# Kernel tuning notes

Measured on AMD Instinct MI355X. Metric: run time of the kernel, lower is better.

Reference implementation:

```python
import jax, jax.numpy as jnp
import numpy as np

K = 1.0      # spring constant
R0 = 1.0     # equilibrium bond length
EPS = 1e-20  # division guard
NUM_GRAPHS = 64


def setup_inputs() -> dict:
    key = jax.random.key(0)
    k1, k2, k3 = jax.random.split(key, 3)
    N, E = 100000, 3200000
    pos = jax.random.normal(k1, (N, 3), dtype=jnp.float32)
    edge_index = jax.random.randint(k2, (2, E), 0, N, dtype=jnp.int64)
    batch = jnp.sort(jax.random.randint(k3, (N,), 0, NUM_GRAPHS, dtype=jnp.int64))
    return {"pos": pos, "edge_index": edge_index, "batch": batch}


def reference(pos, edge_index, batch):
    i, j = edge_index[0], edge_index[1]
    dr = pos[i] - pos[j]                       # (E, 3)
    d = jnp.linalg.norm(dr, axis=1)            # (E,)
    delta = d - R0
    edge_energy = 0.5 * K * delta ** 2         # (E,)
    energy = jax.ops.segment_sum(edge_energy, batch[i], num_segments=NUM_GRAPHS)
    direction = dr / (d + EPS)[:, None]        # (E, 3)
    force_contrib = (K * delta)[:, None] * direction
    forces = jnp.zeros_like(pos).at[i].add(-force_contrib).at[j].add(force_contrib)
    return energy, forces
```

## Files before the change

### kernel.cpp

```cpp
#include <hip/hip_runtime.h>

#define NUM_GRAPHS 64
#define NSC 160
#define SCN 625
#define XPAD 628
#define SB 512
#define CAP 128
#define SEGSTRIDE (NSC * CAP)
#define PBREC 12800
#define BITER 8
#define FSCALE 32768.0f
#define FINV   (1.0f / 32768.0f)

__global__ __launch_bounds__(1024, 8) void bin_kernel(
    const float* __restrict__ pos, const int* __restrict__ batch,
    float4* __restrict__ pos4, float* __restrict__ energy,
    const int* __restrict__ ei,
    unsigned int* __restrict__ recs,
    int* __restrict__ counts,
    int N, int E, int per_block)
{
    __shared__ unsigned int buf[PBREC];
    __shared__ int hist[NSC];
    __shared__ int csr[NSC];
    __shared__ int cursor[NSC];
    __shared__ int scan_s[NSC];

    const int t = threadIdx.x, b = blockIdx.x;
    const int lane = t & 63, w = t >> 6;
    const int e0 = b * per_block, e1 = min(E, e0 + per_block);

    {
        const int gt = b * 1024 + t;
        if (gt < N) {
            float4 v;
            v.x = pos[3 * gt + 0];
            v.y = pos[3 * gt + 1];
            v.z = pos[3 * gt + 2];
            v.w = __int_as_float(batch[gt]);
            pos4[gt] = v;
        }
        if (b == 0 && t < NUM_GRAPHS) energy[t] = 0.f;
    }

    int civ[BITER], cjv[BITER];

    for (int i = t; i < NSC; i += 1024) hist[i] = 0;
    __syncthreads();

    #pragma unroll
    for (int it = 0; it < BITER; ++it) {
        const int e = e0 + t + it * 1024;
        if (e < e1) {
            const int iv = ei[e], jv = ei[E + e];
            civ[it] = iv; cjv[it] = jv;
            atomicAdd(&hist[iv / SCN], 1);
            atomicAdd(&hist[jv / SCN], 1);
        }
    }
    __syncthreads();

    if (t < NSC) scan_s[t] = hist[t];
    __syncthreads();
    for (int d = 1; d < NSC; d <<= 1) {
        int v = 0;
        if (t < NSC && t >= d) v = scan_s[t - d];
        __syncthreads();
        if (t < NSC) scan_s[t] += v;
        __syncthreads();
    }
    if (t < NSC) {
        const int excl = scan_s[t] - hist[t];
        csr[t] = excl;
        cursor[t] = excl;
    }
    __syncthreads();

    #pragma unroll
    for (int it = 0; it < BITER; ++it) {
        const int e = e0 + t + it * 1024;
        if (e < e1) {
            const int iv = civ[it], jv = cjv[it];
            const int si = iv / SCN, sj = jv / SCN;
            const int s1 = atomicAdd(&cursor[si], 1);
            buf[s1] = (unsigned int)(iv - si * SCN) | ((unsigned int)jv << 10) | (1u << 27);
            const int s2 = atomicAdd(&cursor[sj], 1);
            buf[s2] = (unsigned int)(jv - sj * SCN) | ((unsigned int)iv << 10);
        }
    }
    __syncthreads();

    unsigned int* dst0 = recs + (size_t)b * NSC * CAP;
    for (int s = w; s < NSC; s += 16) {
        const int base = csr[s];
        const int cnt  = min(hist[s], CAP);
        for (int k = lane; k < cnt; k += 64)
            dst0[s * CAP + k] = buf[base + k];
        if (lane == 0) counts[b * NSC + s] = cnt;
    }
}

template<int G>
__global__ __launch_bounds__(256, 8) void accumulate_kernel(
    const float4* __restrict__ pos4,
    const unsigned int* __restrict__ recs,
    const int* __restrict__ counts,
    float* __restrict__ energy,
    int* __restrict__ xpart,
    unsigned long long* __restrict__ yzpart)
{
    __shared__ float4 slab[SCN];
    __shared__ __align__(16) int facc_x[XPAD];
    __shared__ __align__(16) unsigned long long facc_yz[XPAD];
    __shared__ float ered[8];

    const int t    = threadIdx.x;
    const int lane = t & 63;
    const int w    = t >> 6;
    const int s    = blockIdx.x % NSC;
    const int g    = blockIdx.x / NSC;

    constexpr int SPB   = SB / G;
    constexpr int SPW   = SPB / 4;
    constexpr int NPASS = (SPW + 7) / 8;

    for (int i = t; i < SCN; i += 256) slab[i] = pos4[s * SCN + i];
    for (int i = 4 * t; i < XPAD; i += 1024) {
        int4 z = {0, 0, 0, 0};
        *(int4*)&facc_x[i] = z;
    }
    for (int i = 4 * t; i < 2 * XPAD; i += 1024) {
        int4 z = {0, 0, 0, 0};
        *(int4*)&((int*)facc_yz)[i] = z;
    }
    __syncthreads();

    const int gmin_i = __float_as_int(slab[0].w);
    float e_lo = 0.f, e_hi = 0.f;

    for (int pass = 0; pass < NPASS; ++pass) {
        const int seg0 = g * SPB + w * SPW + pass * 8;
        int v = (lane < 8) ? counts[(seg0 + lane) * NSC + s] : 0;
        #pragma unroll
        for (int d = 1; d < 8; d <<= 1) {
            const int u = __shfl_up(v, d);
            if (lane >= d) v += u;
        }
        const int b0 = __shfl(v, 0), b1 = __shfl(v, 1), b2 = __shfl(v, 2),
                  b3 = __shfl(v, 3), b4 = __shfl(v, 4), b5 = __shfl(v, 5),
                  b6 = __shfl(v, 6);
        const int tot = __shfl(v, 7);
        const unsigned int* bp = recs + ((size_t)seg0 * NSC + s) * CAP;

        for (int base = 0; base < tot; base += 256) {
            unsigned int rec[4];
            bool  val[4];
            int   a[4];
            float4 pb[4];
            #pragma unroll
            for (int u = 0; u < 4; ++u) {
                const int r = base + lane + (u << 6);
                val[u] = r < tot;
                if (val[u]) {
                    const int k = (r >= b0) + (r >= b1) + (r >= b2) + (r >= b3)
                                + (r >= b4) + (r >= b5) + (r >= b6);
                    int prev = 0;
                    prev = (k > 0) ? b0 : prev; prev = (k > 1) ? b1 : prev;
                    prev = (k > 2) ? b2 : prev; prev = (k > 3) ? b3 : prev;
                    prev = (k > 4) ? b4 : prev; prev = (k > 5) ? b5 : prev;
                    prev = (k > 6) ? b6 : prev;
                    rec[u] = bp[(size_t)k * SEGSTRIDE + (r - prev)];
                }
            }
            #pragma unroll
            for (int u = 0; u < 4; ++u) {
                if (val[u]) {
                    a[u]  = (int)(rec[u] & 1023);
                    pb[u] = pos4[(rec[u] >> 10) & 0x1FFFF];
                }
            }
            #pragma unroll
            for (int u = 0; u < 4; ++u) {
                if (val[u]) {
                    const float4 pa = slab[a[u]];
                    const float dx = pa.x - pb[u].x;
                    const float dy = pa.y - pb[u].y;
                    const float dz = pa.z - pb[u].z;
                    const float r2  = fmaxf(dx*dx + dy*dy + dz*dz, 1e-24f);
                    const float inv = __builtin_amdgcn_rsqf(r2);
                    const float sc  = 1.0f - inv;
                    const int xq = __float2int_rn(-sc * dx * FSCALE);
                    const int yq = __float2int_rn(-sc * dy * FSCALE);
                    const int zq = __float2int_rn(-sc * dz * FSCALE);
                    atomicAdd(&facc_x[a[u]], xq);
                    const unsigned long long pk =
                        ((unsigned long long)(unsigned int)zq << 32)
                        + (unsigned long long)(unsigned int)yq;
                    atomicAdd(&facc_yz[a[u]], pk);
                    if (rec[u] >> 27) {
                        const float delta = r2 * inv - 1.0f;
                        const float e = 0.5f * delta * delta;
                        if (__float_as_int(pa.w) == gmin_i) e_lo += e;
                        else                                e_hi += e;
                    }
                }
            }
        }
    }

    #pragma unroll
    for (int d = 32; d > 0; d >>= 1) {
        e_lo += __shfl_down(e_lo, d);
        e_hi += __shfl_down(e_hi, d);
    }
    if (lane == 0) { ered[2 * w] = e_lo; ered[2 * w + 1] = e_hi; }

    __syncthreads();
    int* xdst = xpart + (size_t)(s * G + g) * XPAD;
    unsigned long long* zdst = yzpart + (size_t)(s * G + g) * XPAD;
    for (int i = t; i < SCN; i += 256) xdst[i] = facc_x[i];
    for (int i = t; i < SCN; i += 256) zdst[i] = facc_yz[i];
    if (t == 0)
        atomicAdd(&energy[__float_as_int(slab[0].w)],
                  ered[0] + ered[2] + ered[4] + ered[6]);
    if (t == 1)
        atomicAdd(&energy[__float_as_int(slab[SCN - 1].w)],
                  ered[1] + ered[3] + ered[5] + ered[7]);
}

template<int G>
__global__ __launch_bounds__(256) void reduce_kernel(
    const int* __restrict__ xpart,
    const unsigned long long* __restrict__ yzpart,
    float* __restrict__ forces, int N)
{
    const int n = blockIdx.x * 256 + threadIdx.x;
    if (n >= N) return;
    const int s = n / SCN, a = n - s * SCN;
    int sx = 0, sy = 0, sz = 0;
    #pragma unroll
    for (int g = 0; g < G; ++g) {
        const size_t p = (size_t)(s * G + g) * XPAD + a;
        sx += xpart[p];
        const unsigned long long v = yzpart[p];
        sy += (int)(unsigned int)(v & 0xffffffffull);
        sz += (int)(unsigned int)(v >> 32);
    }
    forces[3 * n + 0] = (float)sx * FINV;
    forces[3 * n + 1] = (float)sy * FINV;
    forces[3 * n + 2] = (float)sz * FINV;
}

extern "C" void kernel_launch(void* const* d_in, const int* in_sizes, int n_in,
                              void* d_out, int out_size, void* d_ws, size_t ws_size,
                              hipStream_t stream) {
    const float* pos   = (const float*)d_in[0];
    const int*   ei    = (const int*)d_in[1];
    const int*   batch = (const int*)d_in[2];

    const int E = in_sizes[1] / 2;
    const int N = in_sizes[0] / 3;

    float* energy = (float*)d_out;
    float* forces = (float*)d_out + NUM_GRAPHS;

    const int per_block = (E + SB - 1) / SB;

    char* w = (char*)d_ws;
    float4* pos4 = (float4*)w;
    size_t off = (size_t)N * 16;
    unsigned int* recs = (unsigned int*)(w + off);
    off += (size_t)SB * NSC * CAP * 4;
    int* counts = (int*)(w + off);
    off += (size_t)SB * NSC * 4;
    int* xpart = (int*)(w + off);
    const size_t xbytes16 = (size_t)NSC * 16 * XPAD * 4;
    const size_t xbytes8  = (size_t)NSC * 8  * XPAD * 4;

    bin_kernel<<<SB, 1024, 0, stream>>>(pos, batch, pos4, energy,
                                        ei, recs, counts, N, E, per_block);

    const size_t need16 = off + xbytes16 + (size_t)NSC * 16 * XPAD * 8;
    if (ws_size >= need16) {
        unsigned long long* yzpart = (unsigned long long*)((char*)xpart + xbytes16);
        accumulate_kernel<16><<<NSC * 16, 256, 0, stream>>>(
            pos4, recs, counts, energy, xpart, yzpart);
        reduce_kernel<16><<<(N + 255) / 256, 256, 0, stream>>>(
            xpart, yzpart, forces, N);
    } else {
        unsigned long long* yzpart = (unsigned long long*)((char*)xpart + xbytes8);
        accumulate_kernel<8><<<NSC * 8, 256, 0, stream>>>(
            pos4, recs, counts, energy, xpart, yzpart);
        reduce_kernel<8><<<(N + 255) / 256, 256, 0, stream>>>(
            xpart, yzpart, forces, N);
    }
}
```

Baseline: 142.7 us.

## Replace per-group force partials with global atomic accumulation

Each accumulate block now atomically adds its fixed-point force tile into a single global per-node buffer, which the bin kernel zeroes. This replaces writing G partial slabs and summing them in a separate reduce kernel. The final pass becomes a simple coalesced convert over 3N outputs. In exchange it adds global atomic contention (16 groups per node) and always uses G=16 without the workspace-size fallback.

```diff
diff --git a/kernel.cpp b/kernel.cpp
--- a/kernel.cpp
+++ b/kernel.cpp
@@ -15,6 +15,8 @@
 __global__ __launch_bounds__(1024, 8) void bin_kernel(
     const float* __restrict__ pos, const int* __restrict__ batch,
     float4* __restrict__ pos4, float* __restrict__ energy,
+    int* __restrict__ gx,
+    unsigned long long* __restrict__ gyz,
     const int* __restrict__ ei,
     unsigned int* __restrict__ recs,
     int* __restrict__ counts,
@@ -39,6 +41,8 @@
             v.z = pos[3 * gt + 2];
             v.w = __int_as_float(batch[gt]);
             pos4[gt] = v;
+            gx[gt] = 0;
+            gyz[gt] = 0ull;
         }
         if (b == 0 && t < NUM_GRAPHS) energy[t] = 0.f;
     }
@@ -106,8 +110,8 @@
     const unsigned int* __restrict__ recs,
     const int* __restrict__ counts,
     float* __restrict__ energy,
-    int* __restrict__ xpart,
-    unsigned long long* __restrict__ yzpart)
+    int* __restrict__ gx,
+    unsigned long long* __restrict__ gyz)
 {
     __shared__ float4 slab[SCN];
     __shared__ __align__(16) int facc_x[XPAD];
@@ -216,10 +220,8 @@
     if (lane == 0) { ered[2 * w] = e_lo; ered[2 * w + 1] = e_hi; }
 
     __syncthreads();
-    int* xdst = xpart + (size_t)(s * G + g) * XPAD;
-    unsigned long long* zdst = yzpart + (size_t)(s * G + g) * XPAD;
-    for (int i = t; i < SCN; i += 256) xdst[i] = facc_x[i];
-    for (int i = t; i < SCN; i += 256) zdst[i] = facc_yz[i];
+    for (int i = t; i < SCN; i += 256) atomicAdd(&gx[s * SCN + i], facc_x[i]);
+    for (int i = t; i < SCN; i += 256) atomicAdd(&gyz[s * SCN + i], facc_yz[i]);
     if (t == 0)
         atomicAdd(&energy[__float_as_int(slab[0].w)],
                   ered[0] + ered[2] + ered[4] + ered[6]);
@@ -228,27 +230,19 @@
                   ered[1] + ered[3] + ered[5] + ered[7]);
 }
 
-template<int G>
-__global__ __launch_bounds__(256) void reduce_kernel(
-    const int* __restrict__ xpart,
-    const unsigned long long* __restrict__ yzpart,
+__global__ __launch_bounds__(256) void convert_kernel(
+    const int* __restrict__ gx,
+    const unsigned long long* __restrict__ gyz,
     float* __restrict__ forces, int N)
 {
-    const int n = blockIdx.x * 256 + threadIdx.x;
-    if (n >= N) return;
-    const int s = n / SCN, a = n - s * SCN;
-    int sx = 0, sy = 0, sz = 0;
-    #pragma unroll
-    for (int g = 0; g < G; ++g) {
-        const size_t p = (size_t)(s * G + g) * XPAD + a;
-        sx += xpart[p];
-        const unsigned long long v = yzpart[p];
-        sy += (int)(unsigned int)(v & 0xffffffffull);
-        sz += (int)(unsigned int)(v >> 32);
-    }
-    forces[3 * n + 0] = (float)sx * FINV;
-    forces[3 * n + 1] = (float)sy * FINV;
-    forces[3 * n + 2] = (float)sz * FINV;
+    const int idx = blockIdx.x * 256 + threadIdx.x;
+    if (idx >= 3 * N) return;
+    const int n = idx / 3, c = idx - 3 * n;
+    int v;
+    if (c == 0)      v = gx[n];
+    else if (c == 1) v = (int)(unsigned int)(gyz[n] & 0xffffffffull);
+    else             v = (int)(unsigned int)(gyz[n] >> 32);
+    forces[idx] = (float)v * FINV;
 }
 
 extern "C" void kernel_launch(void* const* d_in, const int* in_sizes, int n_in,
@@ -273,25 +267,16 @@
     off += (size_t)SB * NSC * CAP * 4;
     int* counts = (int*)(w + off);
     off += (size_t)SB * NSC * 4;
-    int* xpart = (int*)(w + off);
-    const size_t xbytes16 = (size_t)NSC * 16 * XPAD * 4;
-    const size_t xbytes8  = (size_t)NSC * 8  * XPAD * 4;
-
-    bin_kernel<<<SB, 1024, 0, stream>>>(pos, batch, pos4, energy,
+    int* gx = (int*)(w + off);
+    off += (size_t)N * 4;
+    unsigned long long* gyz = (unsigned long long*)(w + off);
+
+    bin_kernel<<<SB, 1024, 0, stream>>>(pos, batch, pos4, energy, gx, gyz,
                                         ei, recs, counts, N, E, per_block);
 
-    const size_t need16 = off + xbytes16 + (size_t)NSC * 16 * XPAD * 8;
-    if (ws_size >= need16) {
-        unsigned long long* yzpart = (unsigned long long*)((char*)xpart + xbytes16);
-        accumulate_kernel<16><<<NSC * 16, 256, 0, stream>>>(
-            pos4, recs, counts, energy, xpart, yzpart);
-        reduce_kernel<16><<<(N + 255) / 256, 256, 0, stream>>>(
-            xpart, yzpart, forces, N);
-    } else {
-        unsigned long long* yzpart = (unsigned long long*)((char*)xpart + xbytes8);
-        accumulate_kernel<8><<<NSC * 8, 256, 0, stream>>>(
-            pos4, recs, counts, energy, xpart, yzpart);
-        reduce_kernel<8><<<(N + 255) / 256, 256, 0, stream>>>(
-            xpart, yzpart, forces, N);
-    }
-}
+    accumulate_kernel<16><<<NSC * 16, 256, 0, stream>>>(
+        pos4, recs, counts, energy, gx, gyz);
+
+    convert_kernel<<<(3 * N + 255) / 256, 256, 0, stream>>>(
+        gx, gyz, forces, N);
+}
```

Result: slower. 151.5 us (+6.2%).
